# Optimization experiments

Measured on AMD Instinct MI355X. Metric: run time of the kernel, lower is better.

Reference implementation:

```python
import jax, jax.numpy as jnp
import numpy as np

D_MODEL = 2048
N_HEADS = 16
D_HEAD = 128
BATCH = 2
SEQ = 2048


def setup_inputs() -> dict:
    key = jax.random.key(0)
    ks = jax.random.split(key, 5)
    x = jax.random.normal(ks[0], (BATCH, SEQ, D_MODEL), dtype=jnp.float32)
    # fused QKV projection: out features = d_model + 2*d_head
    W_qkv = jax.random.normal(ks[1], (D_MODEL, D_MODEL + 2 * D_HEAD), dtype=jnp.float32) * (D_MODEL ** -0.5)
    b_qkv = jax.random.normal(ks[2], (D_MODEL + 2 * D_HEAD,), dtype=jnp.float32) * 0.02
    W_out = jax.random.normal(ks[3], (D_MODEL, D_MODEL), dtype=jnp.float32) * (D_MODEL ** -0.5)
    b_out = jax.random.normal(ks[4], (D_MODEL,), dtype=jnp.float32) * 0.02
    return {"x": x, "W_qkv": W_qkv, "b_qkv": b_qkv, "W_out": W_out, "b_out": b_out}


def reference(x, W_qkv, b_qkv, W_out, b_out):
    B, S, _ = x.shape
    qkv = jnp.einsum('bsd,de->bse', x, W_qkv) + b_qkv
    q, k, v = jnp.split(qkv, [D_MODEL, D_MODEL + D_HEAD], axis=-1)
    # q: [B, H, S, Dh]; k, v: single shared head [B, S, Dh] (MQA broadcast)
    q = q.reshape(B, S, N_HEADS, D_HEAD).transpose(0, 2, 1, 3)
    scale = 1.0 / jnp.sqrt(jnp.float32(D_HEAD))
    # scores: [B, H, S, S] -- shared K broadcast across heads
    scores = jnp.einsum('bhqd,bkd->bhqk', q, k) * scale
    causal = jnp.tril(jnp.ones((S, S), dtype=bool))
    scores = jnp.where(causal, scores, jnp.finfo(scores.dtype).min)
    attn = jax.nn.softmax(scores, axis=-1)
    out = jnp.einsum('bhqk,bkd->bhqd', attn, v)  # shared V broadcast
    out = out.transpose(0, 2, 1, 3).reshape(B, S, D_MODEL)
    return jnp.einsum('bsd,de->bse', out, W_out) + b_out
```

## Files before the change

### kernel.cpp

```cpp
#include <hip/hip_runtime.h>

#define D_MODEL 2048
#define QKVC 2304
#define DH 128
#define NH 16
#define BATCH 2
#define SEQ 2048
#define MROWS (BATCH*SEQ)

typedef __attribute__((ext_vector_type(4))) float f32x4;
typedef __attribute__((ext_vector_type(16))) float f32x16;
typedef __attribute__((ext_vector_type(8))) short s16x8;
typedef __attribute__((ext_vector_type(8))) __bf16 bf16x8;
typedef __attribute__((ext_vector_type(4))) unsigned int u32x4;

static __device__ __forceinline__ unsigned short f2bf(float f) {
  unsigned int u = __builtin_bit_cast(unsigned int, f);
  u += 0x7fff + ((u >> 16) & 1);
  return (unsigned short)(u >> 16);
}

static __device__ __forceinline__ unsigned int pkbf(float a, float b) {
  unsigned short x = __builtin_bit_cast(unsigned short, (__bf16)a);
  unsigned short y = __builtin_bit_cast(unsigned short, (__bf16)b);
  return (unsigned int)x | ((unsigned int)y << 16);
}

static __device__ __forceinline__ f32x4 mfma16(s16x8 a, s16x8 b, f32x4 c) {
  return __builtin_amdgcn_mfma_f32_16x16x32_bf16(
      __builtin_bit_cast(bf16x8, a), __builtin_bit_cast(bf16x8, b), c, 0, 0, 0);
}

static __device__ __forceinline__ f32x16 mfma32(s16x8 a, s16x8 b, f32x16 c) {
  return __builtin_amdgcn_mfma_f32_32x32x16_bf16(
      __builtin_bit_cast(bf16x8, a), __builtin_bit_cast(bf16x8, b), c, 0, 0, 0);
}

typedef const __attribute__((address_space(1))) void gvoid_t;
typedef __attribute__((address_space(3))) void svoid_t;

static __device__ __forceinline__ void gload_lds16(const void* g, void* l) {
  __builtin_amdgcn_global_load_lds((gvoid_t*)g, (svoid_t*)l, 16, 0, 0);
}

__global__ void cvt_bf16_kernel(const float* __restrict__ in,
                                unsigned short* __restrict__ out, int n4) {
  int i = blockIdx.x * blockDim.x + threadIdx.x;
  int stride = gridDim.x * blockDim.x;
  for (int idx = i; idx < n4; idx += stride) {
    float4 v = ((const float4*)in)[idx];
    ushort4 o;
    o.x = f2bf(v.x); o.y = f2bf(v.y); o.z = f2bf(v.z); o.w = f2bf(v.w);
    ((ushort4*)out)[idx] = o;
  }
}

__global__ void transpose_cvt_kernel(const float* __restrict__ in,
                                     unsigned short* __restrict__ out,
                                     int R, int C) {
  __shared__ float tile[32][33];
  int c0 = blockIdx.x * 32, r0 = blockIdx.y * 32;
  int tx = threadIdx.x, ty = threadIdx.y;
#pragma unroll
  for (int i = 0; i < 4; ++i)
    tile[ty + i*8][tx] = in[(size_t)(r0 + ty + i*8) * C + c0 + tx];
  __syncthreads();
#pragma unroll
  for (int i = 0; i < 4; ++i)
    out[(size_t)(c0 + ty + i*8) * R + r0 + tx] = f2bf(tile[tx][ty + i*8]);
}

__global__ void transpose_v_kernel(const unsigned short* __restrict__ qkv,
                                   unsigned short* __restrict__ VT) {
  __shared__ unsigned short tile[32][33];
  int s0 = blockIdx.x * 32, d0 = blockIdx.y * 32, b = blockIdx.z;
  int tx = threadIdx.x, ty = threadIdx.y;
#pragma unroll
  for (int i = 0; i < 4; ++i)
    tile[ty + i*8][tx] =
        qkv[(size_t)(b*SEQ + s0 + ty + i*8) * QKVC + (D_MODEL + DH) + d0 + tx];
  __syncthreads();
#pragma unroll
  for (int i = 0; i < 4; ++i)
    VT[(size_t)(b*DH + d0 + ty + i*8) * SEQ + s0 + tx] = tile[tx][ty + i*8];
}

template<int OUT_F32>
__global__ __launch_bounds__(256, 2)
void gemm_bt_kernel(const unsigned short* __restrict__ A,
                    const unsigned short* __restrict__ BT,
                    const float* __restrict__ bias,
                    void* __restrict__ Cout,
                    int M, int N, int K) {
  __shared__ unsigned short Al[128*32];
  __shared__ unsigned short Bl[128*32];
  int tid = threadIdx.x;
  int lane = tid & 63, wave = tid >> 6;
  int m0 = blockIdx.y * 128, n0 = blockIdx.x * 128;
  int wr = wave >> 1, wc = wave & 1;
  int fr = lane & 15, fq = lane >> 4;
  f32x4 acc[4][4] = {};

  int c0 = wave * 2;
  int kcol = (lane & 3) * 8;
  int rsub = (lane >> 2);

  for (int k0 = 0; k0 < K; k0 += 32) {
#pragma unroll
    for (int i = 0; i < 2; ++i) {
      int c = c0 + i;
      int row = c*16 + rsub;
      gload_lds16(A  + (size_t)(m0 + row)*K + k0 + kcol, (char*)Al + c*1024);
      gload_lds16(BT + (size_t)(n0 + row)*K + k0 + kcol, (char*)Bl + c*1024);
    }
    __syncthreads();
    s16x8 af[4], bfr[4];
#pragma unroll
    for (int m = 0; m < 4; ++m)
      af[m] = *(const s16x8*)&Al[(wr*64 + m*16 + fr)*32 + fq*8];
#pragma unroll
    for (int n = 0; n < 4; ++n)
      bfr[n] = *(const s16x8*)&Bl[(wc*64 + n*16 + fr)*32 + fq*8];
#pragma unroll
    for (int m = 0; m < 4; ++m)
#pragma unroll
      for (int n = 0; n < 4; ++n)
        acc[m][n] = mfma16(af[m], bfr[n], acc[m][n]);
    __syncthreads();
  }

#pragma unroll
  for (int n = 0; n < 4; ++n) {
    int col = n0 + wc*64 + n*16 + fr;
    float bv = bias[col];
#pragma unroll
    for (int m = 0; m < 4; ++m) {
      int rowb = m0 + wr*64 + m*16 + fq*4;
#pragma unroll
      for (int j = 0; j < 4; ++j) {
        float v = acc[m][n][j] + bv;
        if (OUT_F32) ((float*)Cout)[(size_t)(rowb + j)*N + col] = v;
        else ((unsigned short*)Cout)[(size_t)(rowb + j)*N + col] = f2bf(v);
      }
    }
  }
}

__global__ __launch_bounds__(256, 2)
void mqa_attn_kernel(const unsigned short* __restrict__ qkv,
                     const unsigned short* __restrict__ VT,
                     unsigned short* __restrict__ O) {
  __shared__ unsigned short Kl[2][64*128];
  __shared__ unsigned short Vl[2][128*64];
  int qt = (gridDim.x - 1) - blockIdx.x;
  int hg = blockIdx.y, b = blockIdx.z;
  int tid = threadIdx.x;
  int lane = tid & 63, wid = tid >> 6;
  int fr = lane & 31, hi = lane >> 5;
  int h = hg*4 + wid;
  int q0 = qt*32;
  const float C = 0.12751688f;

#define STAGE(kb_, buf_) do {                                              \
    int kv0_ = (kb_)*64;                                                   \
    _Pragma("unroll")                                                      \
    for (int i_ = 0; i_ < 4; ++i_) {                                       \
      int idx_ = i_*256 + tid;                                             \
      int r_ = idx_ >> 4, c_ = idx_ & 15;                                  \
      gload_lds16(qkv + (size_t)(b*SEQ + kv0_ + r_)*QKVC + D_MODEL         \
                      + ((c_ ^ (r_ & 15)) * 8),                            \
                  (char*)&Kl[buf_][0] + (size_t)idx_*16);                  \
      int d_ = idx_ >> 3, c2_ = idx_ & 7;                                  \
      gload_lds16(VT + (size_t)(b*DH + d_)*SEQ + kv0_ + ((c2_ ^ (d_ & 7))*8), \
                  (char*)&Vl[buf_][0] + (size_t)idx_*16);                  \
    }                                                                      \
  } while (0)

  s16x8 qf[8];
  {
    const unsigned short* qb =
        qkv + (size_t)(b*SEQ + q0 + fr)*QKVC + h*DH + hi*8;
#pragma unroll
    for (int s = 0; s < 8; ++s) qf[s] = *(const s16x8*)(qb + s*16);
  }

  f32x16 oacc[4] = {};
  float m_r = -1.0e30f, l_r = 0.f;

  int nkb = (qt >> 1) + 1;
  STAGE(0, 0);
  __syncthreads();

  for (int kb = 0; kb < nkb; ++kb) {
    int cur = kb & 1;
    if (kb + 1 < nkb) STAGE(kb + 1, cur ^ 1);

    const unsigned short* Kb = &Kl[cur][0];
    const unsigned short* Vb = &Vl[cur][0];
    int kv0 = kb*64;

    f32x16 sfr[2] = {};
    __builtin_amdgcn_s_setprio(1);
#pragma unroll
    for (int t = 0; t < 2; ++t) {
      int row = t*32 + fr;
#pragma unroll
      for (int s = 0; s < 8; ++s) {
        int cc = (s*2 + hi) ^ (fr & 15);
        s16x8 kf = *(const s16x8*)&Kb[row*128 + cc*8];
        sfr[t] = mfma32(kf, qf[s], sfr[t]);
      }
    }
    __builtin_amdgcn_s_setprio(0);

    if (kb == nkb - 1) {
      int q = q0 + fr;
#pragma unroll
      for (int t = 0; t < 2; ++t)
#pragma unroll
        for (int r = 0; r < 16; ++r) {
          int kv = kv0 + t*32 + (r & 3) + 8*(r >> 2) + 4*hi;
          if (kv > q) sfr[t][r] = -1.0e30f;
        }
    }

    float mx[8];
#pragma unroll
    for (int r = 0; r < 8; ++r)
      mx[r] = fmaxf(fmaxf(sfr[0][r], sfr[0][r+8]),
                    fmaxf(sfr[1][r], sfr[1][r+8]));
    float pm = fmaxf(fmaxf(fmaxf(mx[0], mx[4]), fmaxf(mx[1], mx[5])),
                     fmaxf(fmaxf(mx[2], mx[6]), fmaxf(mx[3], mx[7])));
    pm = fmaxf(pm, __shfl_xor(pm, 32));

    bool stable = __all(pm - m_r <= 90.0f) != 0;
    float fac = 1.0f;
    if (!stable) {
      float mnew = fmaxf(m_r, pm);
      fac = exp2f((m_r - mnew) * C);
      m_r = mnew;
    }
    float mC = m_r * C;
#pragma unroll
    for (int t = 0; t < 2; ++t)
#pragma unroll
      for (int r = 0; r < 16; ++r)
        sfr[t][r] = exp2f(__builtin_fmaf(sfr[t][r], C, -mC));

    float sm[8];
#pragma unroll
    for (int r = 0; r < 8; ++r)
      sm[r] = (sfr[0][r] + sfr[0][r+8]) + (sfr[1][r] + sfr[1][r+8]);
    float rs = ((sm[0]+sm[1]) + (sm[2]+sm[3]))
             + ((sm[4]+sm[5]) + (sm[6]+sm[7]));
    rs += __shfl_xor(rs, 32);
    l_r = l_r * fac + rs;

    if (!stable) {
#pragma unroll
      for (int r = 0; r < 16; ++r) {
        int src = (r & 3) + 8*(r >> 2) + 4*hi;
        float fv = __shfl(fac, src);
#pragma unroll
        for (int n2 = 0; n2 < 4; ++n2) oacc[n2][r] *= fv;
      }
    }

#pragma unroll
    for (int t = 0; t < 2; ++t) {
      s16x8 pa[2];
#pragma unroll
      for (int ks = 0; ks < 2; ++ks) {
        unsigned int X0 = pkbf(sfr[t][8*ks+0], sfr[t][8*ks+1]);
        unsigned int X1 = pkbf(sfr[t][8*ks+2], sfr[t][8*ks+3]);
        unsigned int Y0 = pkbf(sfr[t][8*ks+4], sfr[t][8*ks+5]);
        unsigned int Y1 = pkbf(sfr[t][8*ks+6], sfr[t][8*ks+7]);
        unsigned int s0 = __shfl_xor(hi ? X0 : Y0, 32);
        unsigned int s1 = __shfl_xor(hi ? X1 : Y1, 32);
        u32x4 pw;
        pw[0] = hi ? s0 : X0;
        pw[1] = hi ? s1 : X1;
        pw[2] = hi ? Y0 : s0;
        pw[3] = hi ? Y1 : s1;
        pa[ks] = __builtin_bit_cast(s16x8, pw);
      }
      __builtin_amdgcn_s_setprio(1);
#pragma unroll
      for (int n2 = 0; n2 < 4; ++n2) {
        int d = n2*32 + fr;
#pragma unroll
        for (int ks = 0; ks < 2; ++ks) {
          int cc = (t*4 + ks*2 + hi) ^ (d & 7);
          s16x8 vf = *(const s16x8*)&Vb[d*64 + cc*8];
          oacc[n2] = mfma32(pa[ks], vf, oacc[n2]);
        }
      }
      __builtin_amdgcn_s_setprio(0);
    }

    __syncthreads();
  }

  float invl = 1.0f / l_r;
#pragma unroll
  for (int r = 0; r < 16; ++r) {
    int qrow = (r & 3) + 8*(r >> 2) + 4*hi;
    float iv = __shfl(invl, qrow);
    size_t rowoff = (size_t)(b*SEQ + q0 + qrow)*D_MODEL + h*DH;
#pragma unroll
    for (int n2 = 0; n2 < 4; ++n2)
      O[rowoff + n2*32 + fr] = f2bf(oacc[n2][r] * iv);
  }
#undef STAGE
}

extern "C" void kernel_launch(void* const* d_in, const int* in_sizes, int n_in,
                              void* d_out, int out_size, void* d_ws, size_t ws_size,
                              hipStream_t stream) {
  const float* x     = (const float*)d_in[0];
  const float* W_qkv = (const float*)d_in[1];
  const float* b_qkv = (const float*)d_in[2];
  const float* W_out = (const float*)d_in[3];
  const float* b_out = (const float*)d_in[4];
  float* out = (float*)d_out;

  unsigned short* x_bf = (unsigned short*)d_ws;
  unsigned short* WqT  = x_bf + (size_t)MROWS * D_MODEL;
  unsigned short* WoT  = WqT  + (size_t)QKVC * D_MODEL;
  unsigned short* qkvb = WoT  + (size_t)D_MODEL * D_MODEL;
  unsigned short* VTb  = qkvb + (size_t)MROWS * QKVC;
  unsigned short* Ob   = VTb  + (size_t)BATCH * DH * SEQ;

  dim3 tb(32, 8);
  cvt_bf16_kernel<<<2048, 256, 0, stream>>>(x, x_bf, (MROWS * D_MODEL) / 4);
  transpose_cvt_kernel<<<dim3(QKVC/32, D_MODEL/32), tb, 0, stream>>>(W_qkv, WqT, D_MODEL, QKVC);
  transpose_cvt_kernel<<<dim3(D_MODEL/32, D_MODEL/32), tb, 0, stream>>>(W_out, WoT, D_MODEL, D_MODEL);

  gemm_bt_kernel<0><<<dim3(QKVC/128, MROWS/128), 256, 0, stream>>>(
      x_bf, WqT, b_qkv, qkvb, MROWS, QKVC, D_MODEL);

  transpose_v_kernel<<<dim3(SEQ/32, DH/32, BATCH), tb, 0, stream>>>(qkvb, VTb);

  mqa_attn_kernel<<<dim3(SEQ/32, NH/4, BATCH), 256, 0, stream>>>(qkvb, VTb, Ob);

  gemm_bt_kernel<1><<<dim3(D_MODEL/128, MROWS/128), 256, 0, stream>>>(
      Ob, WoT, b_out, out, MROWS, D_MODEL, D_MODEL);
}
```

Measured before the change: 227.4 us.

## Balance causal attention by pairing long and short query tiles per block

Restructures the attention kernel so each 512-thread block handles a pair of query tiles (a long tile and a mirrored short one) split across two 256-thread groups. Each group works through a fixed budget of 17 KV steps: the short tile is finished first, then the remaining KV blocks of the long tile are processed and merged with the other group's partial result via an LDS flash-decoding style combine. This removes the load imbalance of causal masking and halves the grid to 256 uniform blocks. It adds LDS usage, a cross-group merge, and extra register pressure at 512 threads per block.

```diff
diff --git a/kernel.cpp b/kernel.cpp
--- a/kernel.cpp
+++ b/kernel.cpp
@@ -146,59 +146,72 @@
   }
 }
 
-__global__ __launch_bounds__(256, 2)
+__global__ __launch_bounds__(512, 2)
 void mqa_attn_kernel(const unsigned short* __restrict__ qkv,
                      const unsigned short* __restrict__ VT,
                      unsigned short* __restrict__ O) {
-  __shared__ unsigned short Kl[2][64*128];
-  __shared__ unsigned short Vl[2][128*64];
-  int qt = (gridDim.x - 1) - blockIdx.x;
-  int hg = blockIdx.y, b = blockIdx.z;
+  __shared__ unsigned short Kst[2][2][64*128];
+  __shared__ unsigned short Vst[2][2][128*64];
+  int u = blockIdx.x;
+  int b = u >> 7;
+  int hg = (u >> 5) & 3;
+  int x = u & 31;
+  int qtA = 63 - x, qtB = x;
+  int nkbA = (qtA >> 1) + 1, nkbB = (qtB >> 1) + 1;
+  const int G1 = 17;
+  bool hasPart = (nkbA > G1);
+
   int tid = threadIdx.x;
-  int lane = tid & 63, wid = tid >> 6;
+  int grp = tid >> 8;
+  int tg  = tid & 255;
+  int lane = tid & 63;
+  int wid4 = (tid >> 6) & 3;
   int fr = lane & 31, hi = lane >> 5;
-  int h = hg*4 + wid;
-  int q0 = qt*32;
+  int h = hg*4 + wid4;
   const float C = 0.12751688f;
 
-#define STAGE(kb_, buf_) do {                                              \
-    int kv0_ = (kb_)*64;                                                   \
-    _Pragma("unroll")                                                      \
-    for (int i_ = 0; i_ < 4; ++i_) {                                       \
-      int idx_ = i_*256 + tid;                                             \
-      int r_ = idx_ >> 4, c_ = idx_ & 15;                                  \
-      gload_lds16(qkv + (size_t)(b*SEQ + kv0_ + r_)*QKVC + D_MODEL         \
-                      + ((c_ ^ (r_ & 15)) * 8),                            \
-                  (char*)&Kl[buf_][0] + (size_t)idx_*16);                  \
-      int d_ = idx_ >> 3, c2_ = idx_ & 7;                                  \
-      gload_lds16(VT + (size_t)(b*DH + d_)*SEQ + kv0_ + ((c2_ ^ (d_ & 7))*8), \
-                  (char*)&Vl[buf_][0] + (size_t)idx_*16);                  \
-    }                                                                      \
+  auto tile_desc = [&](int g, int st, int& qt, int& kb) -> bool {
+    if (g == 0) { qt = qtA; kb = st; return st < G1; }
+    if (st < nkbB) { qt = qtB; kb = st; return true; }
+    int k2 = G1 + (st - nkbB);
+    qt = qtA; kb = k2;
+    return k2 < nkbA;
+  };
+
+#define STAGE_G(kv0_, Kp_, Vp_) do {                                        \
+    _Pragma("unroll")                                                       \
+    for (int i_ = 0; i_ < 4; ++i_) {                                        \
+      int idx_ = i_*256 + tg;                                               \
+      int r_ = idx_ >> 4, c_ = idx_ & 15;                                   \
+      gload_lds16(qkv + (size_t)(b*SEQ + (kv0_) + r_)*QKVC + D_MODEL        \
+                      + ((c_ ^ (r_ & 15)) * 8),                             \
+                  (char*)(Kp_) + (size_t)idx_*16);                          \
+      int d_ = idx_ >> 3, c2_ = idx_ & 7;                                   \
+      gload_lds16(VT + (size_t)(b*DH + d_)*SEQ + (kv0_) + ((c2_^(d_&7))*8), \
+                  (char*)(Vp_) + (size_t)idx_*16);                          \
+    }                                                                       \
   } while (0)
 
   s16x8 qf[8];
-  {
+  f32x16 oacc[4];
+  float m_r, l_r;
+
+  auto load_q = [&](int qt_) {
     const unsigned short* qb =
-        qkv + (size_t)(b*SEQ + q0 + fr)*QKVC + h*DH + hi*8;
+        qkv + (size_t)(b*SEQ + qt_*32 + fr)*QKVC + h*DH + hi*8;
 #pragma unroll
     for (int s = 0; s < 8; ++s) qf[s] = *(const s16x8*)(qb + s*16);
-  }
-
-  f32x16 oacc[4] = {};
-  float m_r = -1.0e30f, l_r = 0.f;
-
-  int nkb = (qt >> 1) + 1;
-  STAGE(0, 0);
-  __syncthreads();
-
-  for (int kb = 0; kb < nkb; ++kb) {
-    int cur = kb & 1;
-    if (kb + 1 < nkb) STAGE(kb + 1, cur ^ 1);
-
-    const unsigned short* Kb = &Kl[cur][0];
-    const unsigned short* Vb = &Vl[cur][0];
-    int kv0 = kb*64;
-
+  };
+  auto reset_state = [&]() {
+#pragma unroll
+    for (int n2 = 0; n2 < 4; ++n2)
+#pragma unroll
+      for (int e = 0; e < 16; ++e) oacc[n2][e] = 0.f;
+    m_r = -1.0e30f; l_r = 0.f;
+  };
+
+  auto do_tile = [&](const unsigned short* Kb, const unsigned short* Vb,
+                     int q0, int kv0) {
     f32x16 sfr[2] = {};
     __builtin_amdgcn_s_setprio(1);
 #pragma unroll
@@ -213,7 +226,7 @@
     }
     __builtin_amdgcn_s_setprio(0);
 
-    if (kb == nkb - 1) {
+    if (kv0 + 63 > q0) {
       int q = q0 + fr;
 #pragma unroll
       for (int t = 0; t < 2; ++t)
@@ -297,21 +310,90 @@
       }
       __builtin_amdgcn_s_setprio(0);
     }
-
+  };
+
+  auto do_epilogue = [&](int qt_) {
+    float invl = 1.0f / l_r;
+#pragma unroll
+    for (int r = 0; r < 16; ++r) {
+      int qrow = (r & 3) + 8*(r >> 2) + 4*hi;
+      float iv = __shfl(invl, qrow);
+      size_t rowoff = (size_t)(b*SEQ + qt_*32 + qrow)*D_MODEL + h*DH;
+#pragma unroll
+      for (int n2 = 0; n2 < 4; ++n2)
+        O[rowoff + n2*32 + fr] = f2bf(oacc[n2][r] * iv);
+    }
+  };
+
+  load_q(grp ? qtB : qtA);
+  reset_state();
+
+  {
+    int qts, kbs;
+    tile_desc(grp, 0, qts, kbs);
+    STAGE_G(kbs*64, &Kst[grp][0][0], &Vst[grp][0][0]);
+  }
+  __syncthreads();
+
+  for (int st = 0; st < G1; ++st) {
+    int qtn, kbn;
+    if (tile_desc(grp, st + 1, qtn, kbn))
+      STAGE_G(kbn*64, &Kst[grp][(st+1)&1][0], &Vst[grp][(st+1)&1][0]);
+
+    int qtc, kbc;
+    if (tile_desc(grp, st, qtc, kbc)) {
+      do_tile(&Kst[grp][st&1][0], &Vst[grp][st&1][0], qtc*32, kbc*64);
+      if (grp == 1 && st == nkbB - 1) {
+        do_epilogue(qtB);
+        load_q(qtA);
+        reset_state();
+      }
+    }
     __syncthreads();
   }
 
-  float invl = 1.0f / l_r;
-#pragma unroll
-  for (int r = 0; r < 16; ++r) {
-    int qrow = (r & 3) + 8*(r >> 2) + 4*hi;
-    float iv = __shfl(invl, qrow);
-    size_t rowoff = (size_t)(b*SEQ + q0 + qrow)*D_MODEL + h*DH;
-#pragma unroll
-    for (int n2 = 0; n2 < 4; ++n2)
-      O[rowoff + n2*32 + fr] = f2bf(oacc[n2][r] * iv);
-  }
-#undef STAGE
+  if (grp == 1 && hasPart) {
+    float* Dls = (float*)&Kst[0][0][0];
+    float* Mls = (float*)&Vst[0][0][0];
+#pragma unroll
+    for (int r = 0; r < 16; ++r) {
+      int q = (r & 3) + 8*(r >> 2) + 4*hi;
+#pragma unroll
+      for (int n2 = 0; n2 < 4; ++n2)
+        Dls[(wid4*32 + q)*128 + n2*32 + fr] = oacc[n2][r];
+    }
+    if (hi == 0) {
+      Mls[wid4*32 + fr] = m_r;
+      Mls[128 + wid4*32 + fr] = l_r;
+    }
+  }
+  __syncthreads();
+
+  if (grp == 0) {
+    if (hasPart) {
+      const float* Dls = (const float*)&Kst[0][0][0];
+      const float* Mls = (const float*)&Vst[0][0][0];
+      float m2 = Mls[wid4*32 + fr], l2 = Mls[128 + wid4*32 + fr];
+      float mm = fmaxf(m_r, m2);
+      float fA = exp2f((m_r - mm) * C);
+      float fB = exp2f((m2 - mm) * C);
+      float inv = 1.0f / (fA*l_r + fB*l2);
+#pragma unroll
+      for (int r = 0; r < 16; ++r) {
+        int q = (r & 3) + 8*(r >> 2) + 4*hi;
+        float fAs = __shfl(fA, q), fBs = __shfl(fB, q), invs = __shfl(inv, q);
+        size_t rowoff = (size_t)(b*SEQ + qtA*32 + q)*D_MODEL + h*DH;
+#pragma unroll
+        for (int n2 = 0; n2 < 4; ++n2) {
+          float o2 = Dls[(wid4*32 + q)*128 + n2*32 + fr];
+          O[rowoff + n2*32 + fr] = f2bf((fAs*oacc[n2][r] + fBs*o2) * invs);
+        }
+      }
+    } else {
+      do_epilogue(qtA);
+    }
+  }
+#undef STAGE_G
 }
 
 extern "C" void kernel_launch(void* const* d_in, const int* in_sizes, int n_in,
@@ -341,7 +423,7 @@
 
   transpose_v_kernel<<<dim3(SEQ/32, DH/32, BATCH), tb, 0, stream>>>(qkvb, VTb);
 
-  mqa_attn_kernel<<<dim3(SEQ/32, NH/4, BATCH), 256, 0, stream>>>(qkvb, VTb, Ob);
+  mqa_attn_kernel<<<dim3(256), 512, 0, stream>>>(qkvb, VTb, Ob);
 
   gemm_bt_kernel<1><<<dim3(D_MODEL/128, MROWS/128), 256, 0, stream>>>(
       Ob, WoT, b_out, out, MROWS, D_MODEL, D_MODEL);
```

Result: faster. 194.8 us (median of 4 runs) (-14.3%).
